# Performance work log

Hardware: AMD Instinct MI355X
Metric: run time of the kernel (lower is better)

Reference implementation:

```python
import jax, jax.numpy as jnp
import numpy as np

# Qwen3.5 GatedDeltaNet config (Qwen3-Next linear-attention block)
HIDDEN = 2048
HV, HK = 32, 16          # value heads, key heads (GQA rep = 2)
DK, DV = 128, 128        # key/value head dims
KCONV = 4                # causal depthwise conv kernel
KEY_DIM = HK * DK        # 2048
VAL_DIM = HV * DV        # 4096
CONV_DIM = 2 * KEY_DIM + VAL_DIM  # 8192
EPS = 1e-6


def setup_inputs() -> dict:
    key = jax.random.key(0)
    ks = jax.random.split(key, 9)
    B, S = 2, 1024
    def w(k, shape, sc=0.02):
        return jax.random.normal(k, shape, jnp.float32) * sc
    return {
        "hidden_states": jax.random.normal(ks[0], (B, S, HIDDEN), jnp.float32),
        "conv_w": w(ks[1], (CONV_DIM, 1, KCONV), 0.1),   # depthwise conv1d weight (groups=CONV_DIM, no bias)
        "w_qkv": w(ks[2], (HIDDEN, CONV_DIM)),
        "w_z": w(ks[3], (HIDDEN, VAL_DIM)),
        "w_b": w(ks[4], (HIDDEN, HV)),
        "w_a": w(ks[5], (HIDDEN, HV)),
        "w_out": w(ks[6], (VAL_DIM, HIDDEN)),
        "dt_bias": jnp.ones((HV,), jnp.float32),
        "A_log": jnp.log(jax.random.uniform(ks[7], (HV,), jnp.float32, 1e-3, 16.0)),
        "norm_w": jnp.ones((DV,), jnp.float32),
    }


def _l2norm(x):
    return x / jnp.sqrt(jnp.sum(x * x, axis=-1, keepdims=True) + 1e-6)


def reference(hidden_states, conv_w, w_qkv, w_z, w_b, w_a, w_out, dt_bias, A_log, norm_w):
    B, S, _ = hidden_states.shape
    # input projections
    mixed = hidden_states @ w_qkv                     # [B,S,CONV_DIM]
    z = (hidden_states @ w_z).reshape(B, S, HV, DV)   # gate for RMSNormGated
    b = hidden_states @ w_b                           # [B,S,HV]
    a = hidden_states @ w_a                           # [B,S,HV]

    # causal depthwise conv1d (left pad K-1), then SiLU
    x = mixed.transpose(0, 2, 1)                      # [B,C,S]
    y = jax.lax.conv_general_dilated(
        x, conv_w, window_strides=(1,), padding=[(KCONV - 1, 0)],
        dimension_numbers=("NCH", "OIH", "NCH"), feature_group_count=CONV_DIM)
    mixed = jax.nn.silu(y).transpose(0, 2, 1)         # [B,S,CONV_DIM]

    q, k, v = jnp.split(mixed, [KEY_DIM, 2 * KEY_DIM], axis=-1)
    q = q.reshape(B, S, HK, DK)
    k = k.reshape(B, S, HK, DK)
    v = v.reshape(B, S, HV, DV)

    beta = jax.nn.sigmoid(b)                                    # [B,S,HV]
    g = -jnp.exp(A_log) * jax.nn.softplus(a + dt_bias)          # [B,S,HV], log-decay <= 0

    rep = HV // HK
    q = jnp.repeat(q, rep, axis=2)                              # [B,S,HV,DK]
    k = jnp.repeat(k, rep, axis=2)

    # use_qk_l2norm_in_kernel=True, then standard 1/sqrt(dk) scaling on q
    q = _l2norm(q) * (DK ** -0.5)
    k = _l2norm(k)

    # gated delta-rule recurrence over time (state S: [B,HV,DK,DV])
    qt = q.transpose(1, 0, 2, 3)
    kt = k.transpose(1, 0, 2, 3)
    vt = v.transpose(1, 0, 2, 3)
    gt = g.transpose(1, 0, 2)
    bt = beta.transpose(1, 0, 2)

    S0 = jnp.zeros((B, HV, DK, DV), jnp.float32)

    def step(Sm, inp):
        q_, k_, v_, g_, b_ = inp
        Sm = Sm * jnp.exp(g_)[..., None, None]                  # gated decay
        kv = jnp.einsum('bhk,bhkv->bhv', k_, Sm)                # k^T S (current memory readout)
        delta = (v_ - kv) * b_[..., None]                       # delta-rule update, scaled by beta
        Sm = Sm + jnp.einsum('bhk,bhv->bhkv', k_, delta)        # rank-1 write
        o = jnp.einsum('bhk,bhkv->bhv', q_, Sm)                 # query readout
        return Sm, o

    _, o = jax.lax.scan(step, S0, (qt, kt, vt, gt, bt))
    o = o.transpose(1, 0, 2, 3)                                 # [B,S,HV,DV]

    # RMSNormGated over head_v_dim: gate with silu(z), then RMSNorm
    og = o * jax.nn.silu(z)
    var = jnp.mean(og * og, axis=-1, keepdims=True)
    on = og * jax.lax.rsqrt(var + EPS) * norm_w

    return on.reshape(B, S, VAL_DIM) @ w_out                    # [B,S,HIDDEN]
```

## Files before the change

kernel.cpp:

```cpp
#include <hip/hip_runtime.h>
#include <hip/hip_bf16.h>
#include <cstdint>

#define HIDDEN   2048
#define HV       32
#define HK       16
#define DK       128
#define DV       128
#define KEY_DIM  2048
#define VAL_DIM  4096
#define CONV_DIM 8192
#define NTOK     2048
#define SEQ      1024
#define N1       12288
#define C_CH     64
#define NCHK     (SEQ / C_CH)

typedef __attribute__((ext_vector_type(4))) float f4_t;
typedef __attribute__((ext_vector_type(2))) float f2_t;
typedef __attribute__((ext_vector_type(8))) short bf8_t;
typedef __attribute__((ext_vector_type(16))) float f16acc;
typedef __attribute__((ext_vector_type(4))) unsigned short u16x4;
typedef __attribute__((ext_vector_type(8))) unsigned short u16x8;
typedef __attribute__((ext_vector_type(2))) uint32_t u32x2;
typedef __attribute__((ext_vector_type(4))) uint32_t u32x4;

__device__ __forceinline__ unsigned short f2bf(float f) {
    union { float f; uint32_t u; } a; a.f = f;
    uint32_t u = a.u;
    return (unsigned short)((u + 0x7fff + ((u >> 16) & 1)) >> 16);
}
__device__ __forceinline__ float bf2f(unsigned short h) {
    uint32_t u = ((uint32_t)h) << 16;
    union { uint32_t u; float f; } a; a.u = u;
    return a.f;
}
__device__ __forceinline__ bf8_t lds_frag(const unsigned short* p) {
    u32x2 a = *(const u32x2*)p;
    u32x2 b = *(const u32x2*)(p + 4);
    u32x4 w = {a[0], a[1], b[0], b[1]};
    return __builtin_bit_cast(bf8_t, w);
}

__global__ __launch_bounds__(256) void k_cast_hs(const float* __restrict__ hs,
                                                 unsigned short* __restrict__ out) {
    int i = blockIdx.x * 256 + threadIdx.x;
    f4_t v = ((const f4_t*)hs)[i];
    u16x4 o;
    o[0] = f2bf(v[0]); o[1] = f2bf(v[1]); o[2] = f2bf(v[2]); o[3] = f2bf(v[3]);
    ((u16x4*)out)[i] = o;
}

__global__ __launch_bounds__(256) void k_trans_w1(const float* __restrict__ w_qkv,
                                                  const float* __restrict__ w_z,
                                                  unsigned short* __restrict__ w1t) {
    __shared__ float tile[32][33];
    int tx = threadIdx.x & 31, ty = threadIdx.x >> 5;
    int n0 = blockIdx.x * 32, k0 = blockIdx.y * 32;
    int n = n0 + tx;
#pragma unroll
    for (int i = 0; i < 4; i++) {
        int k = k0 + ty + i * 8;
        float v = (n < CONV_DIM) ? w_qkv[(size_t)k * CONV_DIM + n]
                                 : w_z[(size_t)k * VAL_DIM + (n - CONV_DIM)];
        tile[ty + i * 8][tx] = v;
    }
    __syncthreads();
#pragma unroll
    for (int i = 0; i < 4; i++)
        w1t[(size_t)(n0 + ty + i * 8) * HIDDEN + k0 + tx] = f2bf(tile[tx][ty + i * 8]);
}

__global__ __launch_bounds__(256) void k_trans(const float* __restrict__ src,
                                               unsigned short* __restrict__ dst,
                                               int K, int N) {
    __shared__ float tile[32][33];
    int tx = threadIdx.x & 31, ty = threadIdx.x >> 5;
    int n0 = blockIdx.x * 32, k0 = blockIdx.y * 32;
#pragma unroll
    for (int i = 0; i < 4; i++)
        tile[ty + i * 8][tx] = src[(size_t)(k0 + ty + i * 8) * N + n0 + tx];
    __syncthreads();
#pragma unroll
    for (int i = 0; i < 4; i++)
        dst[(size_t)(n0 + ty + i * 8) * K + k0 + tx] = f2bf(tile[tx][ty + i * 8]);
}

__global__ __launch_bounds__(256, 2) void k_gemm_bt(const unsigned short* __restrict__ A,
                                                    const unsigned short* __restrict__ B,
                                                    float* __restrict__ C, int K, int N) {
    __shared__ unsigned short lA[128 * 32];
    __shared__ unsigned short lB[128 * 32];
    int tid = threadIdx.x;
    int wave = tid >> 6, lane = tid & 63;
    int m0 = blockIdx.x * 128, n0 = blockIdx.y * 128;
    int wm = wave & 1, wn = wave >> 1;
    f4_t acc[4][4];
#pragma unroll
    for (int i = 0; i < 4; i++)
#pragma unroll
        for (int j = 0; j < 4; j++) acc[i][j] = (f4_t){0.f, 0.f, 0.f, 0.f};
    int srow = wave * 16 + (lane >> 2);
    int scol = (lane & 3) * 8;
    int quad = lane >> 4, lrow = lane & 15;

    for (int k0 = 0; k0 < K; k0 += 32) {
        const unsigned short* gA0 = A + (size_t)(m0 + srow) * K + k0 + scol;
        const unsigned short* gA1 = A + (size_t)(m0 + 64 + srow) * K + k0 + scol;
        const unsigned short* gB0 = B + (size_t)(n0 + srow) * K + k0 + scol;
        const unsigned short* gB1 = B + (size_t)(n0 + 64 + srow) * K + k0 + scol;
        __syncthreads();
        __builtin_amdgcn_global_load_lds((const __attribute__((address_space(1))) void*)gA0,
            (__attribute__((address_space(3))) void*)(&lA[wave * 512]), 16, 0, 0);
        __builtin_amdgcn_global_load_lds((const __attribute__((address_space(1))) void*)gA1,
            (__attribute__((address_space(3))) void*)(&lA[2048 + wave * 512]), 16, 0, 0);
        __builtin_amdgcn_global_load_lds((const __attribute__((address_space(1))) void*)gB0,
            (__attribute__((address_space(3))) void*)(&lB[wave * 512]), 16, 0, 0);
        __builtin_amdgcn_global_load_lds((const __attribute__((address_space(1))) void*)gB1,
            (__attribute__((address_space(3))) void*)(&lB[2048 + wave * 512]), 16, 0, 0);
        __syncthreads();
        bf8_t af[4], bfv[4];
#pragma unroll
        for (int i = 0; i < 4; i++) {
            af[i]  = *(const bf8_t*)&lA[(wm * 64 + i * 16 + lrow) * 32 + quad * 8];
            bfv[i] = *(const bf8_t*)&lB[(wn * 64 + i * 16 + lrow) * 32 + quad * 8];
        }
#pragma unroll
        for (int i = 0; i < 4; i++)
#pragma unroll
            for (int j = 0; j < 4; j++)
                acc[i][j] = __builtin_amdgcn_mfma_f32_16x16x32_bf16(af[i], bfv[j], acc[i][j], 0, 0, 0);
    }
#pragma unroll
    for (int i = 0; i < 4; i++) {
        int row_b = m0 + wm * 64 + i * 16 + quad * 4;
#pragma unroll
        for (int j = 0; j < 4; j++) {
            int col = n0 + wn * 64 + j * 16 + lrow;
#pragma unroll
            for (int r = 0; r < 4; r++)
                C[(size_t)(row_b + r) * N + col] = acc[i][j][r];
        }
    }
}

#define BG_TOK 4
__global__ __launch_bounds__(256) void k_beta_g(const float* __restrict__ hs,
                                                const float* __restrict__ w_b,
                                                const float* __restrict__ w_a,
                                                const float* __restrict__ dt_bias,
                                                const float* __restrict__ A_log,
                                                float* __restrict__ beta,
                                                float* __restrict__ gval) {
    __shared__ float rows[BG_TOK * HIDDEN];
    __shared__ float part[BG_TOK][64][17];
    int t = threadIdx.x;
    int tok0 = blockIdx.x * BG_TOK;
    {
        const f4_t* src = (const f4_t*)(hs + (size_t)tok0 * HIDDEN);
        f4_t* dst = (f4_t*)rows;
#pragma unroll
        for (int u = 0; u < BG_TOK * HIDDEN / 4 / 256; u++)
            dst[t + u * 256] = src[t + u * 256];
    }
    __syncthreads();
    int hq = t & 15, kp = t >> 4;
    int h0 = hq * 4;
    const float* wsrc = (h0 < 32) ? (w_b + h0) : (w_a + (h0 - 32));
    f4_t acc[BG_TOK];
#pragma unroll
    for (int x = 0; x < BG_TOK; x++) acc[x] = (f4_t){0.f, 0.f, 0.f, 0.f};
    int kbase = kp * 128;
#pragma unroll 4
    for (int i = 0; i < 128; i++) {
        int k = kbase + i;
        f4_t wv = *(const f4_t*)(wsrc + (size_t)k * 32);
#pragma unroll
        for (int x = 0; x < BG_TOK; x++) {
            float r = rows[x * HIDDEN + k];
            acc[x][0] += wv[0] * r;
            acc[x][1] += wv[1] * r;
            acc[x][2] += wv[2] * r;
            acc[x][3] += wv[3] * r;
        }
    }
#pragma unroll
    for (int x = 0; x < BG_TOK; x++)
#pragma unroll
        for (int e = 0; e < 4; e++)
            part[x][h0 + e][kp] = acc[x][e];
    __syncthreads();
    int x = t >> 6, h = t & 63;
    float s = 0.f;
#pragma unroll
    for (int k2 = 0; k2 < 16; k2++) s += part[x][h][k2];
    int tok = tok0 + x;
    if (h < 32) {
        beta[tok * 32 + h] = 1.f / (1.f + expf(-s));
    } else {
        int hh = h - 32;
        float xx = s + dt_bias[hh];
        float sp = (xx > 20.f) ? xx : log1pf(expf(xx));
        gval[tok * 32 + hh] = -expf(A_log[hh]) * sp;
    }
}

#define CCH 32
#define NCHC (SEQ / CCH)
__global__ __launch_bounds__(256) void k_halo(const float* __restrict__ mixed,
                                              float* __restrict__ halo) {
    int id = blockIdx.x * 256 + threadIdx.x;
    int c = id & 8191;
    int r = id >> 13;
    int tap = r % 3;
    int ck = (r / 3) % (NCHC - 1);
    int b = r / (3 * (NCHC - 1));
    int s = (ck + 1) * CCH - 1 - tap;
    halo[id] = mixed[(size_t)(b * SEQ + s) * N1 + c];
}

__global__ __launch_bounds__(256) void k_conv(float* __restrict__ mixed,
                                              const float* __restrict__ cw,
                                              const float* __restrict__ halo) {
    int id = blockIdx.x * 256 + threadIdx.x;
    int c = id & 8191;
    int r = id >> 13;
    int chunk = r & (NCHC - 1), b = r >> 5;
    int s0 = chunk * CCH;
    float w0 = cw[c * 4 + 0], w1 = cw[c * 4 + 1], w2 = cw[c * 4 + 2], w3 = cw[c * 4 + 3];
    float xm1, xm2, xm3;
    if (chunk == 0) {
        xm1 = xm2 = xm3 = 0.f;
    } else {
        const float* hp = halo + (size_t)(b * (NCHC - 1) + chunk - 1) * 3 * 8192;
        xm1 = hp[0 * 8192 + c]; xm2 = hp[1 * 8192 + c]; xm3 = hp[2 * 8192 + c];
    }
    float* col = mixed + (size_t)(b * SEQ + s0) * N1 + c;
#pragma unroll
    for (int s = 0; s < CCH; s++) {
        float x = col[(size_t)s * N1];
        float y = w3 * x + w2 * xm1 + w1 * xm2 + w0 * xm3;
        y = y / (1.f + expf(-y));
        col[(size_t)s * N1] = y;
        xm3 = xm2; xm2 = xm1; xm1 = x;
    }
}

__global__ __launch_bounds__(256) void k_l2norm(float* __restrict__ mixed) {
    int tok = blockIdx.x, t = threadIdx.x;
    int vec = t >> 3, ln = t & 7;
    int off = (vec < 16) ? vec * 128 : 2048 + (vec - 16) * 128;
    float* p = mixed + (size_t)tok * N1 + off + ln * 16;
    f4_t x0 = ((f4_t*)p)[0], x1 = ((f4_t*)p)[1], x2 = ((f4_t*)p)[2], x3 = ((f4_t*)p)[3];
    float ss = 0.f;
#pragma unroll
    for (int i = 0; i < 4; i++) ss += x0[i]*x0[i] + x1[i]*x1[i] + x2[i]*x2[i] + x3[i]*x3[i];
    ss += __shfl_xor(ss, 1); ss += __shfl_xor(ss, 2); ss += __shfl_xor(ss, 4);
    float sc = 1.f / sqrtf(ss + 1e-6f);
    if (vec < 16) sc *= 0.08838834764831845f;
#pragma unroll
    for (int i = 0; i < 4; i++) { x0[i]*=sc; x1[i]*=sc; x2[i]*=sc; x3[i]*=sc; }
    ((f4_t*)p)[0] = x0; ((f4_t*)p)[1] = x1; ((f4_t*)p)[2] = x2; ((f4_t*)p)[3] = x3;
}

__global__ __launch_bounds__(256, 2) void k_prep(const float* __restrict__ mixed,
                                                 const float* __restrict__ beta,
                                                 const float* __restrict__ gval,
                                                 unsigned short* __restrict__ Pg,
                                                 unsigned short* __restrict__ KbTg,
                                                 unsigned short* __restrict__ Qbg,
                                                 unsigned short* __restrict__ Wg,
                                                 float* __restrict__ Ug,
                                                 float* __restrict__ Lamg) {
    __shared__ unsigned short lK[64 * 132];
    __shared__ unsigned short lQ[64 * 132];
    __shared__ float lM[64 * 66];
    __shared__ float lG[64], lLam[64], lBeta[64], lKsc[64];

    int blk = blockIdx.x;
    int c = blk & 15, h = (blk >> 4) & 31, b = blk >> 9;
    int hk = h >> 1;
    int t = threadIdx.x;
    int wave = t >> 6, lane = t & 63, half = lane >> 5, lm = lane & 31;
    int s0 = c * C_CH;

    const float* qptr = mixed + (size_t)(b * SEQ) * N1 + hk * 128;
    const float* kptr = qptr + 2048;

    {
        int i = t >> 2, c0 = (t & 3) * 32;
        const float* kr = kptr + (size_t)(s0 + i) * N1 + c0;
        const float* qr = qptr + (size_t)(s0 + i) * N1 + c0;
        unsigned short* dK = &lK[i * 132 + c0];
        unsigned short* dQ = &lQ[i * 132 + c0];
#pragma unroll
        for (int u = 0; u < 8; u++) {
            f4_t kv = ((const f4_t*)kr)[u];
            f4_t qv = ((const f4_t*)qr)[u];
            u16x4 ks, qs;
#pragma unroll
            for (int e = 0; e < 4; e++) { ks[e] = f2bf(kv[e]); qs[e] = f2bf(qv[e]); }
            *(u16x4*)(dK + u * 4) = ks;
            *(u16x4*)(dQ + u * 4) = qs;
        }
        if (t < 64) {
            float gv = gval[(size_t)(b * SEQ + s0 + t) * 32 + h];
            float bv = beta[(size_t)(b * SEQ + s0 + t) * 32 + h];
            float x = gv;
#pragma unroll
            for (int d = 1; d < 64; d <<= 1) {
                float y = __shfl_up(x, d);
                if (t >= d) x += y;
            }
            float Gc = __shfl(x, 63);
            lG[t] = x; lLam[t] = expf(x); lBeta[t] = bv; lKsc[t] = expf(Gc - x);
        }
    }
    __syncthreads();

    size_t bhc = (size_t)(b * 32 + h) * 16 + c;
    size_t bkc = (size_t)(b * 16 + hk) * 16 + c;

    for (int job = wave; job < 6; job += 4) {
        int isP = job >= 3 ? 1 : 0;
        int jj = job - (isP ? 3 : 0);
        int ib = (jj == 0) ? 0 : 1;
        int jb = (jj == 2) ? 1 : 0;
        const unsigned short* Ab = isP ? lQ : lK;
        f16acc acc;
#pragma unroll
        for (int r = 0; r < 16; r++) acc[r] = 0.f;
        int arow = ib * 32 + lm, brow = jb * 32 + lm;
#pragma unroll
        for (int k0 = 0; k0 < 128; k0 += 16) {
            bf8_t a = lds_frag(&Ab[arow * 132 + k0 + half * 8]);
            bf8_t bb = lds_frag(&lK[brow * 132 + k0 + half * 8]);
            acc = __builtin_amdgcn_mfma_f32_32x32x16_bf16(a, bb, acc, 0, 0, 0);
        }
        int j = jb * 32 + lm;
        float Gj = lG[j];
#pragma unroll
        for (int r = 0; r < 16; r++) {
            int ml = (r & 3) + 8 * (r >> 2) + 4 * half;
            int i = ib * 32 + ml;
            float f = expf(lG[i] - Gj);
            if (isP) {
                Pg[bhc * 4096 + i * 64 + j] = f2bf((j <= i) ? acc[r] * f : 0.f);
            } else {
                if (j < i) lM[i * 66 + j] = acc[r] * lBeta[i] * f;
            }
        }
    }
#pragma unroll
    for (int u = 0; u < 4; u++) {
        int e = t * 4 + u;
        Pg[bhc * 4096 + (e >> 5) * 64 + 32 + (e & 31)] = 0;
    }

    if ((h & 1) == 0) {
        int i = t >> 2, c0 = (t & 3) * 32;
#pragma unroll
        for (int u = 0; u < 8; u++)
            *(u16x4*)&Qbg[bkc * 8192 + i * 128 + c0 + u * 4] = *(const u16x4*)&lQ[i * 132 + c0 + u * 4];
    }

    {
        int dk = t >> 1, i0 = (t & 1) * 32;
        unsigned short tmp[32];
#pragma unroll
        for (int ii = 0; ii < 32; ii++) {
            int i = i0 + ii;
            tmp[ii] = f2bf(bf2f(lK[i * 132 + dk]) * lKsc[i]);
        }
#pragma unroll
        for (int u = 0; u < 4; u++) {
            u16x8 w;
#pragma unroll
            for (int j = 0; j < 8; j++) w[j] = tmp[u * 8 + j];
            *(u16x8*)&KbTg[bhc * 8192 + dk * 64 + i0 + u * 8] = w;
        }
    }
    if (t < 64) Lamg[bhc * 64 + t] = lLam[t];

    __syncthreads();

    {
        float x[64];
        if (t < 128) {
            const float* vcol = mixed + (size_t)(b * SEQ + s0) * N1 + 4096 + h * 128 + t;
#pragma unroll
            for (int il = 0; il < 64; il++) x[il] = lBeta[il] * vcol[(size_t)il * N1];
        } else {
            int dk = t - 128;
#pragma unroll
            for (int il = 0; il < 64; il++) x[il] = lBeta[il] * lLam[il] * bf2f(lK[il * 132 + dk]);
        }
#pragma unroll
        for (int il = 1; il < 64; il++)
#pragma unroll
            for (int j = 0; j < il; j++)
                x[il] -= lM[il * 66 + j] * x[j];
        if (t < 128) {
            float* up = Ug + (size_t)(b * SEQ + s0) * 4096 + h * 128 + t;
#pragma unroll
            for (int il = 0; il < 64; il++) up[(size_t)il * 4096] = x[il];
        } else {
            unsigned short* wp = Wg + bhc * 8192 + (t - 128);
#pragma unroll
            for (int il = 0; il < 64; il++) wp[il * 128] = f2bf(-x[il]);
        }
    }
}

__global__ __launch_bounds__(256, 1) void k_state(const unsigned short* __restrict__ Wg,
                                                  const unsigned short* __restrict__ Pg,
                                                  const unsigned short* __restrict__ KbTg,
                                                  const unsigned short* __restrict__ Qbg,
                                                  const float* __restrict__ Lamg,
                                                  float* __restrict__ o) {
    __shared__ unsigned short lSt[32 * 132];
    __shared__ unsigned short lDt[32 * 68];

    int blk = blockIdx.x;
    int vs = blk & 3, h = (blk >> 2) & 31, b = blk >> 7;
    int hk = h >> 1;
    int t = threadIdx.x;
    int wave = t >> 6, lane = t & 63, half = lane >> 5, lm = lane & 31;
    int ib = wave & 1;

    for (int i = t; i < 32 * 132; i += 256) lSt[i] = 0;
    f16acc sacc;
#pragma unroll
    for (int r = 0; r < 16; r++) sacc[r] = 0.f;
    __syncthreads();

    for (int c = 0; c < NCHK; c++) {
        int s0 = c * C_CH;
        size_t bhc = (size_t)(b * 32 + h) * 16 + c;
        size_t bkc = (size_t)(b * 16 + hk) * 16 + c;

        const unsigned short* Ag = (wave < 2) ? (Wg + bhc * 8192) : (Qbg + bkc * 8192);
        bf8_t afr[8];
#pragma unroll
        for (int kk = 0; kk < 8; kk++)
            afr[kk] = *(const bf8_t*)&Ag[(ib * 32 + lm) * 128 + kk * 16 + half * 8];
        bf8_t ktfr[4];
#pragma unroll
        for (int u = 0; u < 4; u++)
            ktfr[u] = *(const bf8_t*)&KbTg[bhc * 8192 + (wave * 32 + lm) * 64 + u * 16 + half * 8];
        bf8_t pfr[4];
        f4_t lamv[4];
        if (wave >= 2) {
#pragma unroll
            for (int u = 0; u < 4; u++)
                pfr[u] = *(const bf8_t*)&Pg[bhc * 4096 + (ib * 32 + lm) * 64 + u * 16 + half * 8];
#pragma unroll
            for (int q = 0; q < 4; q++)
                lamv[q] = *(const f4_t*)&Lamg[bhc * 64 + ib * 32 + q * 8 + half * 4];
        }
        float lamC = Lamg[bhc * 64 + 63];

        f16acc wacc;
        if (wave < 2) {
            const float* up = o + (size_t)(b * SEQ + s0 + ib * 32) * 4096 + h * 128 + vs * 32 + lm;
#pragma unroll
            for (int r = 0; r < 16; r++) {
                int ml = (r & 3) + 8 * (r >> 2) + 4 * half;
                wacc[r] = up[(size_t)ml * 4096];
            }
        } else {
#pragma unroll
            for (int r = 0; r < 16; r++) wacc[r] = 0.f;
        }
#pragma unroll
        for (int kk = 0; kk < 8; kk++) {
            bf8_t bb = lds_frag(&lSt[lm * 132 + kk * 16 + half * 8]);
            wacc = __builtin_amdgcn_mfma_f32_32x32x16_bf16(afr[kk], bb, wacc, 0, 0, 0);
        }
        if (wave < 2) {
#pragma unroll
            for (int r = 0; r < 16; r++) {
                int ml = (r & 3) + 8 * (r >> 2) + 4 * half;
                lDt[lm * 68 + ib * 32 + ml] = f2bf(wacc[r]);
            }
        }
        __syncthreads();

        if (wave >= 2) {
#pragma unroll
            for (int r = 0; r < 16; r++) wacc[r] *= lamv[r >> 2][r & 3];
#pragma unroll
            for (int u = 0; u < 4; u++) {
                bf8_t bb = lds_frag(&lDt[lm * 68 + u * 16 + half * 8]);
                wacc = __builtin_amdgcn_mfma_f32_32x32x16_bf16(pfr[u], bb, wacc, 0, 0, 0);
            }
#pragma unroll
            for (int r = 0; r < 16; r++) {
                int ml = (r & 3) + 8 * (r >> 2) + 4 * half;
                o[(size_t)(b * SEQ + s0 + ib * 32 + ml) * 4096 + h * 128 + vs * 32 + lm] = wacc[r];
            }
        }
#pragma unroll
        for (int r = 0; r < 16; r++) sacc[r] *= lamC;
#pragma unroll
        for (int u = 0; u < 4; u++) {
            bf8_t bb = lds_frag(&lDt[lm * 68 + u * 16 + half * 8]);
            sacc = __builtin_amdgcn_mfma_f32_32x32x16_bf16(ktfr[u], bb, sacc, 0, 0, 0);
        }
#pragma unroll
        for (int r = 0; r < 16; r++) {
            int ml = (r & 3) + 8 * (r >> 2) + 4 * half;
            lSt[lm * 132 + 32 * wave + ml] = f2bf(sacc[r]);
        }
        __syncthreads();
    }
}

__global__ __launch_bounds__(256) void k_gnorm(const float* __restrict__ o,
                                               const float* __restrict__ mixed,
                                               const float* __restrict__ norm_w,
                                               unsigned short* __restrict__ on) {
    int tok = blockIdx.x, t = threadIdx.x;
    int hh = t >> 3, ln = t & 7;
    const f4_t* op = (const f4_t*)(o + (size_t)tok * 4096 + hh * 128 + ln * 16);
    const f4_t* zp = (const f4_t*)(mixed + (size_t)tok * N1 + 8192 + hh * 128 + ln * 16);
    float og[16];
    float ss = 0.f;
#pragma unroll
    for (int i = 0; i < 4; i++) {
        f4_t ov = op[i], zv = zp[i];
#pragma unroll
        for (int j = 0; j < 4; j++) {
            float z = zv[j];
            float g = ov[j] * (z / (1.f + expf(-z)));
            og[i * 4 + j] = g;
            ss += g * g;
        }
    }
    ss += __shfl_xor(ss, 1); ss += __shfl_xor(ss, 2); ss += __shfl_xor(ss, 4);
    float r = 1.f / sqrtf(ss * (1.f / 128.f) + 1e-6f);
    unsigned short* onp = on + (size_t)tok * 4096 + hh * 128 + ln * 16;
    u16x8 a, bb;
#pragma unroll
    for (int j = 0; j < 8; j++) a[j] = f2bf(og[j] * r * norm_w[ln * 16 + j]);
#pragma unroll
    for (int j = 0; j < 8; j++) bb[j] = f2bf(og[8 + j] * r * norm_w[ln * 16 + 8 + j]);
    ((u16x8*)onp)[0] = a;
    ((u16x8*)onp)[1] = bb;
}

extern "C" void kernel_launch(void* const* d_in, const int* in_sizes, int n_in,
                              void* d_out, int out_size, void* d_ws, size_t ws_size,
                              hipStream_t stream) {
    const float* hs      = (const float*)d_in[0];
    const float* conv_w  = (const float*)d_in[1];
    const float* w_qkv   = (const float*)d_in[2];
    const float* w_z     = (const float*)d_in[3];
    const float* w_b     = (const float*)d_in[4];
    const float* w_a     = (const float*)d_in[5];
    const float* w_out   = (const float*)d_in[6];
    const float* dt_bias = (const float*)d_in[7];
    const float* A_log   = (const float*)d_in[8];
    const float* norm_w  = (const float*)d_in[9];
    float* out = (float*)d_out;

    char* ws = (char*)d_ws;
    unsigned short* hs_bf = (unsigned short*)ws; ws += (size_t)NTOK * HIDDEN * 2;
    unsigned short* w1t   = (unsigned short*)ws; ws += (size_t)N1 * HIDDEN * 2;
    unsigned short* wot   = (unsigned short*)ws; ws += (size_t)HIDDEN * VAL_DIM * 2;
    float* mixed          = (float*)ws;          ws += (size_t)NTOK * N1 * 4;
    float* beta           = (float*)ws;          ws += (size_t)NTOK * 32 * 4;
    float* gval           = (float*)ws;          ws += (size_t)NTOK * 32 * 4;
    float* halo           = (float*)ws;          ws += (size_t)2 * (NCHC - 1) * 3 * 8192 * 4;
    float* o_buf          = (float*)ws;          ws += (size_t)NTOK * VAL_DIM * 4;
    unsigned short* on_bf = (unsigned short*)ws; ws += (size_t)NTOK * VAL_DIM * 2;

    char* al = (char*)hs_bf;
    unsigned short* Wg    = (unsigned short*)al; al += (size_t)1024 * 8192 * 2;
    unsigned short* Pg    = (unsigned short*)al; al += (size_t)1024 * 4096 * 2;
    unsigned short* KbTg  = (unsigned short*)al; al += (size_t)1024 * 8192 * 2;
    unsigned short* Qbg   = (unsigned short*)al; al += (size_t)512 * 8192 * 2;
    float* Lamg           = (float*)halo;

    k_cast_hs<<<dim3(NTOK * HIDDEN / 4 / 256), 256, 0, stream>>>(hs, hs_bf);
    k_trans_w1<<<dim3(N1 / 32, HIDDEN / 32), 256, 0, stream>>>(w_qkv, w_z, w1t);
    k_trans<<<dim3(HIDDEN / 32, VAL_DIM / 32), 256, 0, stream>>>(w_out, wot, VAL_DIM, HIDDEN);
    k_gemm_bt<<<dim3(NTOK / 128, N1 / 128), 256, 0, stream>>>(hs_bf, w1t, mixed, HIDDEN, N1);
    k_beta_g<<<dim3(NTOK / BG_TOK), 256, 0, stream>>>(hs, w_b, w_a, dt_bias, A_log, beta, gval);
    k_halo<<<dim3(2 * (NCHC - 1) * 3 * 8192 / 256), 256, 0, stream>>>(mixed, halo);
    k_conv<<<dim3(2 * NCHC * 8192 / 256), 256, 0, stream>>>(mixed, conv_w, halo);
    k_l2norm<<<dim3(NTOK), 256, 0, stream>>>(mixed);
    k_prep<<<dim3(1024), 256, 0, stream>>>(mixed, beta, gval, Pg, KbTg, Qbg, Wg, o_buf, Lamg);
    k_state<<<dim3(256), 256, 0, stream>>>(Wg, Pg, KbTg, Qbg, Lamg, o_buf);
    k_gnorm<<<dim3(NTOK), 256, 0, stream>>>(o_buf, mixed, norm_w, on_bf);
    k_gemm_bt<<<dim3(NTOK / 128, HIDDEN / 128), 256, 0, stream>>>(on_bf, wot, out, VAL_DIM, HIDDEN);
}
```

Before: 602.4 us.

## Double-buffer GEMM LDS tiles and swizzle workgroup-to-tile mapping

The bf16 GEMM kernel now uses two LDS buffers per operand and prefetches the next K-slice with global_load_lds while MFMAs run on the current one, which drops one barrier per iteration. It also remaps workgroup IDs in groups of eight so that concurrently running blocks share A/B tiles in cache. The swizzle hardcodes 16 M-tiles (M=2048), which ties the kernel to this problem shape. LDS use doubles, which could reduce occupancy.

```diff
diff --git a/kernel.cpp b/kernel.cpp
--- a/kernel.cpp
+++ b/kernel.cpp
@@ -89,11 +89,14 @@
 __global__ __launch_bounds__(256, 2) void k_gemm_bt(const unsigned short* __restrict__ A,
                                                     const unsigned short* __restrict__ B,
                                                     float* __restrict__ C, int K, int N) {
-    __shared__ unsigned short lA[128 * 32];
-    __shared__ unsigned short lB[128 * 32];
+    __shared__ unsigned short lA[2][128 * 32];
+    __shared__ unsigned short lB[2][128 * 32];
     int tid = threadIdx.x;
     int wave = tid >> 6, lane = tid & 63;
-    int m0 = blockIdx.x * 128, n0 = blockIdx.y * 128;
+    int nwg = gridDim.x * gridDim.y;
+    int lid = blockIdx.y * gridDim.x + blockIdx.x;
+    int swz = (lid & 7) * (nwg >> 3) + (lid >> 3);
+    int m0 = (swz & 15) * 128, n0 = (swz >> 4) * 128;
     int wm = wave & 1, wn = wave >> 1;
     f4_t acc[4][4];
 #pragma unroll
@@ -104,33 +107,44 @@
     int scol = (lane & 3) * 8;
     int quad = lane >> 4, lrow = lane & 15;
 
+    const unsigned short* gA0 = A + (size_t)(m0 + srow) * K + scol;
+    const unsigned short* gA1 = A + (size_t)(m0 + 64 + srow) * K + scol;
+    const unsigned short* gB0 = B + (size_t)(n0 + srow) * K + scol;
+    const unsigned short* gB1 = B + (size_t)(n0 + 64 + srow) * K + scol;
+
+#define GEMM_STAGE(buf, k0)                                                                        \
+    do {                                                                                           \
+        __builtin_amdgcn_global_load_lds((const __attribute__((address_space(1))) void*)(gA0 + (k0)), \
+            (__attribute__((address_space(3))) void*)(&lA[buf][wave * 512]), 16, 0, 0);            \
+        __builtin_amdgcn_global_load_lds((const __attribute__((address_space(1))) void*)(gA1 + (k0)), \
+            (__attribute__((address_space(3))) void*)(&lA[buf][2048 + wave * 512]), 16, 0, 0);     \
+        __builtin_amdgcn_global_load_lds((const __attribute__((address_space(1))) void*)(gB0 + (k0)), \
+            (__attribute__((address_space(3))) void*)(&lB[buf][wave * 512]), 16, 0, 0);            \
+        __builtin_amdgcn_global_load_lds((const __attribute__((address_space(1))) void*)(gB1 + (k0)), \
+            (__attribute__((address_space(3))) void*)(&lB[buf][2048 + wave * 512]), 16, 0, 0);     \
+    } while (0)
+
+    GEMM_STAGE(0, 0);
+    __syncthreads();
+
+    int cur = 0;
     for (int k0 = 0; k0 < K; k0 += 32) {
-        const unsigned short* gA0 = A + (size_t)(m0 + srow) * K + k0 + scol;
-        const unsigned short* gA1 = A + (size_t)(m0 + 64 + srow) * K + k0 + scol;
-        const unsigned short* gB0 = B + (size_t)(n0 + srow) * K + k0 + scol;
-        const unsigned short* gB1 = B + (size_t)(n0 + 64 + srow) * K + k0 + scol;
-        __syncthreads();
-        __builtin_amdgcn_global_load_lds((const __attribute__((address_space(1))) void*)gA0,
-            (__attribute__((address_space(3))) void*)(&lA[wave * 512]), 16, 0, 0);
-        __builtin_amdgcn_global_load_lds((const __attribute__((address_space(1))) void*)gA1,
-            (__attribute__((address_space(3))) void*)(&lA[2048 + wave * 512]), 16, 0, 0);
-        __builtin_amdgcn_global_load_lds((const __attribute__((address_space(1))) void*)gB0,
-            (__attribute__((address_space(3))) void*)(&lB[wave * 512]), 16, 0, 0);
-        __builtin_amdgcn_global_load_lds((const __attribute__((address_space(1))) void*)gB1,
-            (__attribute__((address_space(3))) void*)(&lB[2048 + wave * 512]), 16, 0, 0);
-        __syncthreads();
+        if (k0 + 32 < K) GEMM_STAGE(cur ^ 1, k0 + 32);
         bf8_t af[4], bfv[4];
 #pragma unroll
         for (int i = 0; i < 4; i++) {
-            af[i]  = *(const bf8_t*)&lA[(wm * 64 + i * 16 + lrow) * 32 + quad * 8];
-            bfv[i] = *(const bf8_t*)&lB[(wn * 64 + i * 16 + lrow) * 32 + quad * 8];
+            af[i]  = *(const bf8_t*)&lA[cur][(wm * 64 + i * 16 + lrow) * 32 + quad * 8];
+            bfv[i] = *(const bf8_t*)&lB[cur][(wn * 64 + i * 16 + lrow) * 32 + quad * 8];
         }
 #pragma unroll
         for (int i = 0; i < 4; i++)
 #pragma unroll
             for (int j = 0; j < 4; j++)
                 acc[i][j] = __builtin_amdgcn_mfma_f32_16x16x32_bf16(af[i], bfv[j], acc[i][j], 0, 0, 0);
-    }
+        __syncthreads();
+        cur ^= 1;
+    }
+#undef GEMM_STAGE
 #pragma unroll
     for (int i = 0; i < 4; i++) {
         int row_b = m0 + wm * 64 + i * 16 + quad * 4;
```

Result: faster. 574.8 us (-4.6%).
